# Kernel optimization log

Hardware: AMD Instinct MI355X
Metric: run time of the kernel (lower is better)

The kernel has to match this reference:

```python
import jax, jax.numpy as jnp
import numpy as np

N_NODES = 100000
N_EDGES = 1600000
N_GRAPHS = 512
F_IN = 20
HID = 128
OUT = HID // 2


def _glorot(key, shape):
    fan_in, fan_out = shape[0], shape[1]
    lim = float(np.sqrt(6.0 / (fan_in + fan_out)))
    return jax.random.uniform(key, shape, jnp.float32, -lim, lim)


def setup_inputs() -> dict:
    key = jax.random.key(0)
    ks = jax.random.split(key, 12)
    x = jax.random.normal(ks[0], (N_NODES, F_IN), jnp.float32)
    edge_index = jax.random.randint(ks[1], (2, N_EDGES), 0, N_NODES, dtype=jnp.int64)
    batch = jnp.sort(jax.random.randint(ks[2], (N_NODES,), 0, N_GRAPHS, dtype=jnp.int64))
    return {
        "x": x,
        "edge_index": edge_index,
        "batch": batch,
        "W1": _glorot(ks[3], (F_IN, HID)), "b1": jnp.zeros((HID,), jnp.float32),
        "W2": _glorot(ks[4], (HID, HID)), "b2": jnp.zeros((HID,), jnp.float32),
        "W3": _glorot(ks[5], (HID, HID)), "b3": jnp.zeros((HID,), jnp.float32),
        "Wout": _glorot(ks[6], (HID, OUT)), "bout": jnp.zeros((OUT,), jnp.float32),
    }


def _gcn_conv(x, W, b, src, dst, num_nodes):
    # PyG GCNConv: x' = D^{-1/2} (A + I) D^{-1/2} X W + b (self-loops already in src/dst)
    xw = x @ W                                                  # [N, H]
    ones = jnp.ones(src.shape[0], dtype=xw.dtype)
    deg = jax.ops.segment_sum(ones, dst, num_segments=num_nodes)
    dinv = jnp.where(deg > 0, jax.lax.rsqrt(deg), 0.0)          # [N]
    norm = dinv[src] * dinv[dst]                                # [E+N]
    msg = xw[src] * norm[:, None]                               # gather + scale
    return jax.ops.segment_sum(msg, dst, num_segments=num_nodes) + b


def reference(x, edge_index, batch, W1, b1, W2, b2, W3, b3, Wout, bout):
    num_nodes = x.shape[0]
    loops = jnp.arange(num_nodes, dtype=edge_index.dtype)
    src = jnp.concatenate([edge_index[0], loops])
    dst = jnp.concatenate([edge_index[1], loops])

    h = jax.nn.relu(_gcn_conv(x, W1, b1, src, dst, num_nodes))
    h = jax.nn.relu(_gcn_conv(h, W2, b2, src, dst, num_nodes))
    h = jax.nn.relu(_gcn_conv(h, W3, b3, src, dst, num_nodes))

    # global_mean_pool over graph ids
    sums = jax.ops.segment_sum(h, batch, num_segments=N_GRAPHS)
    counts = jax.ops.segment_sum(jnp.ones(num_nodes, h.dtype), batch, num_segments=N_GRAPHS)
    pooled = sums / jnp.maximum(counts, 1.0)[:, None]           # [G, H]
    return pooled @ Wout + bout                                 # [G, H//2]
```

## Files before the change

### kernel.cpp

```cpp
#include <hip/hip_runtime.h>
#include <hip/hip_fp16.h>

#define N_NODES 100000
#define N_EDGES 1600000
#define N_GRAPHS 512
#define F_IN 20
#define HID 128
#define OUT_F 64

#define BUCKETS 256
#define SPAN 391
#define BCAP 7000
#define EPB 2048

typedef _Float16 half8_t __attribute__((ext_vector_type(8)));
typedef float f32x4_t __attribute__((ext_vector_type(4)));

__device__ inline float4 h4_to_f4(uint2 u) {
    __half2 h0 = *(__half2*)&u.x;
    __half2 h1 = *(__half2*)&u.y;
    float2 f0 = __half22float2(h0);
    float2 f1 = __half22float2(h1);
    return make_float4(f0.x, f0.y, f1.x, f1.y);
}

__global__ __launch_bounds__(256) void partition(const int* __restrict__ src,
                                                 const int* __restrict__ dst,
                                                 int* __restrict__ bpairs,
                                                 int* cur256) {
    __shared__ int lcnt[4][BUCKETS];
    __shared__ int woff[4][BUCKETS];
    int t = threadIdx.x;
    int wv = t >> 6;
    for (int i = t; i < 4 * BUCKETS; i += 256) ((int*)lcnt)[i] = 0;
    __syncthreads();
    int base = blockIdx.x * EPB;
    int myb[8], myp[8], myr[8];
#pragma unroll
    for (int i = 0; i < 8; ++i) {
        int e = base + i * 256 + t;
        int b = -1, p = 0, rk = 0;
        if (e < N_EDGES) {
            int s = src[e], d = dst[e];
            b = d / SPAN;
            p = (s << 9) | (d - b * SPAN);
            rk = atomicAdd(&lcnt[wv][b], 1);
        }
        myb[i] = b; myp[i] = p; myr[i] = rk;
    }
    __syncthreads();
    {
        int c0 = lcnt[0][t], c1 = lcnt[1][t], c2 = lcnt[2][t], c3 = lcnt[3][t];
        int gb = atomicAdd(&cur256[t], c0 + c1 + c2 + c3);
        woff[0][t] = gb;
        woff[1][t] = gb + c0;
        woff[2][t] = gb + c0 + c1;
        woff[3][t] = gb + c0 + c1 + c2;
    }
    __syncthreads();
#pragma unroll
    for (int i = 0; i < 8; ++i) {
        int b = myb[i];
        if (b >= 0) {
            int p = woff[wv][b] + myr[i];
            if (p < BCAP) bpairs[(size_t)b * BCAP + p] = myp[i];
        }
    }
}

__global__ __launch_bounds__(256) void csr_build(const int* __restrict__ bpairs,
                                                 const int* __restrict__ cur256,
                                                 int* __restrict__ row_st,
                                                 int* __restrict__ csr,
                                                 const float* __restrict__ x,
                                                 __half* __restrict__ Xs) {
    __shared__ int ocnt[SPAN];
    __shared__ int sc[512];
    __shared__ int cur[SPAN];
    __shared__ int sbase;
    int b = blockIdx.x, t = threadIdx.x;

    int myc = cur256[t];
    sc[t] = myc;
    __syncthreads();
    for (int o = 1; o < BUCKETS; o <<= 1) {
        int v = (t >= o) ? sc[t - o] : 0;
        __syncthreads();
        sc[t] += v;
        __syncthreads();
    }
    if (t == b) sbase = sc[t] - myc;
    if (b == BUCKETS - 1 && t == 0) row_st[N_NODES] = N_EDGES;

    int n0 = b * SPAN;
    int span = N_NODES - n0; if (span > SPAN) span = SPAN;
    for (int i = t; i < SPAN; i += 256) ocnt[i] = 0;
    __syncthreads();

    int n = cur256[b];
    const int* p = bpairs + (size_t)b * BCAP;
    for (int i = t; i < n; i += 256) atomicAdd(&ocnt[p[i] & 511], 1);
    __syncthreads();
    sc[t]       = (t < span) ? ocnt[t] : 0;
    sc[t + 256] = (t + 256 < span) ? ocnt[t + 256] : 0;
    __syncthreads();
    for (int o = 1; o < 512; o <<= 1) {
        int a0 = (t >= o) ? sc[t - o] : 0;
        int a1 = sc[t + 256 - o];
        __syncthreads();
        sc[t] += a0;
        sc[t + 256] += a1;
        __syncthreads();
    }
    int base = sbase;
    for (int i = t; i < span; i += 256) {
        int start = sc[i] - ocnt[i];
        row_st[n0 + i] = base + start;
        cur[i] = start;
    }
    __syncthreads();
    for (int i = t; i < n; i += 256) {
        int e = p[i];
        int lp = atomicAdd(&cur[e & 511], 1);
        csr[base + lp] = e >> 9;
    }
    for (int i = t; i < span * 32; i += 256) {
        int nl = i >> 5, f = i & 31;
        float v = (f < F_IN) ? x[(size_t)(n0 + nl) * F_IN + f] : 0.f;
        float di = rsqrtf((float)(ocnt[nl] + 1));
        Xs[(size_t)(n0 + nl) * 32 + f] = __float2half(di * v);
    }
}

__global__ __launch_bounds__(256) void layer1(const __half* __restrict__ Xs,
                                              const int* __restrict__ row_st,
                                              const int* __restrict__ csr,
                                              const float* __restrict__ W,
                                              const float* __restrict__ bias,
                                              __half* __restrict__ H) {
    __shared__ float Wlds[F_IN * HID];
    __shared__ float Alds[16 * F_IN];
    const int t = threadIdx.x;
    const int node0 = blockIdx.x * 16;

    for (int i = t; i < F_IN * HID; i += 256) Wlds[i] = W[i];

    const int g = t >> 5;
    const int l = t & 31;
    const int hw = l >> 4, l16 = l & 15;
    const __half2* X2 = (const __half2*)Xs;
    for (int k2 = 0; k2 < 2; ++k2) {
        int nn = node0 + g * 2 + k2;
        int r0 = row_st[nn], r1 = row_st[nn + 1];
        float2 acc = make_float2(0.f, 0.f);
        if (hw == 0) {
            float2 f = __half22float2(X2[(size_t)nn * 16 + l16]);
            acc = f;
        }
        int r = r0 + hw;
        for (; r + 2 < r1; r += 4) {
            float2 f0 = __half22float2(X2[(size_t)csr[r] * 16 + l16]);
            float2 f1 = __half22float2(X2[(size_t)csr[r + 2] * 16 + l16]);
            acc.x += f0.x + f1.x;
            acc.y += f0.y + f1.y;
        }
        if (r < r1) {
            float2 f = __half22float2(X2[(size_t)csr[r] * 16 + l16]);
            acc.x += f.x; acc.y += f.y;
        }
        acc.x += __shfl_xor(acc.x, 16);
        acc.y += __shfl_xor(acc.y, 16);
        if (hw == 0 && l16 < 10) {
            float di = rsqrtf((float)(r1 - r0 + 1));
            Alds[(g * 2 + k2) * F_IN + l16 * 2]     = di * acc.x;
            Alds[(g * 2 + k2) * F_IN + l16 * 2 + 1] = di * acc.y;
        }
    }
    __syncthreads();

    const int h4 = (t & 31) * 4;
    float4 b4 = *(const float4*)&bias[h4];
    float4 acc0 = b4;
    float4 acc1 = b4;
#pragma unroll
    for (int kk = 0; kk < F_IN; ++kk) {
        float a0 = Alds[(g * 2) * F_IN + kk];
        float a1 = Alds[(g * 2 + 1) * F_IN + kk];
        float4 w = *(const float4*)&Wlds[kk * HID + h4];
        acc0.x = fmaf(a0, w.x, acc0.x);
        acc0.y = fmaf(a0, w.y, acc0.y);
        acc0.z = fmaf(a0, w.z, acc0.z);
        acc0.w = fmaf(a0, w.w, acc0.w);
        acc1.x = fmaf(a1, w.x, acc1.x);
        acc1.y = fmaf(a1, w.y, acc1.y);
        acc1.z = fmaf(a1, w.z, acc1.z);
        acc1.w = fmaf(a1, w.w, acc1.w);
    }
    {
        __half2 h0 = __floats2half2_rn(acc0.x, acc0.y);
        __half2 h1 = __floats2half2_rn(acc0.z, acc0.w);
        uint2 u; u.x = *(unsigned*)&h0; u.y = *(unsigned*)&h1;
        ((uint2*)H)[(node0 + g * 2) * 32 + (h4 >> 2)] = u;
    }
    {
        __half2 h0 = __floats2half2_rn(acc1.x, acc1.y);
        __half2 h1 = __floats2half2_rn(acc1.z, acc1.w);
        uint2 u; u.x = *(unsigned*)&h0; u.y = *(unsigned*)&h1;
        ((uint2*)H)[(node0 + g * 2 + 1) * 32 + (h4 >> 2)] = u;
    }
}

__global__ __launch_bounds__(256) void gemm_mfma(const __half* __restrict__ H,
                                                 const float* __restrict__ W,
                                                 const int* __restrict__ row_st,
                                                 __half* __restrict__ T) {
    __shared__ _Float16 Whi[64 * 128];
    __shared__ _Float16 Wlo[64 * 128];
    const int t = threadIdx.x;
    const int c0 = (blockIdx.x & 1) * 64;

    for (int i = t; i < 128 * 64; i += 256) {
        int k = i >> 6, c = i & 63;
        float w = W[k * HID + c0 + c];
        _Float16 hi = (_Float16)w;
        _Float16 lo = (_Float16)((w - (float)hi) * 2048.0f);
        int addr = c * 128 + (((k >> 3) ^ (c & 15)) << 3) + (k & 7);
        Whi[addr] = hi;
        Wlo[addr] = lo;
    }
    __syncthreads();

    const int wv = t >> 6;
    const int l  = t & 63;
    const int lr = l & 15;
    const int lq = l >> 4;

    for (int rep = 0; rep < 4; ++rep) {
        int strip = ((blockIdx.x >> 1) * 4 + wv) * 4 + rep;
        if (strip >= N_NODES / 16) continue;
        int n0 = strip * 16;

        f32x4_t acc[4], acl[4];
#pragma unroll
        for (int ct = 0; ct < 4; ++ct) { acc[ct] = (f32x4_t){0,0,0,0}; acl[ct] = (f32x4_t){0,0,0,0}; }

#pragma unroll
        for (int kc = 0; kc < 4; ++kc) {
            half8_t a = *(const half8_t*)(H + (size_t)(n0 + lr) * 128 + kc * 32 + lq * 8);
#pragma unroll
            for (int j = 0; j < 8; ++j) a[j] = a[j] > (_Float16)0 ? a[j] : (_Float16)0;
            int g = kc * 4 + lq;
#pragma unroll
            for (int ct = 0; ct < 4; ++ct) {
                int c = ct * 16 + lr;
                int addr = c * 128 + ((g ^ lr) << 3);
                half8_t bh = *(const half8_t*)&Whi[addr];
                half8_t bl = *(const half8_t*)&Wlo[addr];
                acc[ct] = __builtin_amdgcn_mfma_f32_16x16x32_f16(a, bh, acc[ct], 0, 0, 0);
                acl[ct] = __builtin_amdgcn_mfma_f32_16x16x32_f16(a, bl, acl[ct], 0, 0, 0);
            }
        }

        int r0 = n0 + lq * 4;
#pragma unroll
        for (int r = 0; r < 4; ++r) {
            int row = r0 + r;
            float d = rsqrtf((float)(row_st[row + 1] - row_st[row] + 1));
#pragma unroll
            for (int ct = 0; ct < 4; ++ct) {
                float v = (acc[ct][r] + acl[ct][r] * 4.8828125e-4f) * d;
                T[(size_t)row * 128 + c0 + ct * 16 + lr] = __float2half(v);
            }
        }
    }
}

__global__ __launch_bounds__(256) void gather_range(const __half* __restrict__ A,
                                                    const int* __restrict__ row_st,
                                                    const int* __restrict__ csr,
                                                    const float* __restrict__ bias,
                                                    __half* __restrict__ B) {
    int t = threadIdx.x;
    int n = blockIdx.x * 8 + (t >> 5);
    int l = t & 31;
    int r0 = row_st[n], r1 = row_st[n + 1];
    float di = rsqrtf((float)(r1 - r0 + 1));
    const uint2* Af = (const uint2*)A;
    float4 acc = h4_to_f4(Af[n * 32 + l]);
    int r = r0;
    for (; r + 7 < r1; r += 8) {
        int s0 = csr[r],     s1 = csr[r + 1], s2 = csr[r + 2], s3 = csr[r + 3];
        int s4 = csr[r + 4], s5 = csr[r + 5], s6 = csr[r + 6], s7 = csr[r + 7];
        float4 v0 = h4_to_f4(Af[s0 * 32 + l]);
        float4 v1 = h4_to_f4(Af[s1 * 32 + l]);
        float4 v2 = h4_to_f4(Af[s2 * 32 + l]);
        float4 v3 = h4_to_f4(Af[s3 * 32 + l]);
        float4 v4 = h4_to_f4(Af[s4 * 32 + l]);
        float4 v5 = h4_to_f4(Af[s5 * 32 + l]);
        float4 v6 = h4_to_f4(Af[s6 * 32 + l]);
        float4 v7 = h4_to_f4(Af[s7 * 32 + l]);
        acc.x += ((v0.x + v1.x) + (v2.x + v3.x)) + ((v4.x + v5.x) + (v6.x + v7.x));
        acc.y += ((v0.y + v1.y) + (v2.y + v3.y)) + ((v4.y + v5.y) + (v6.y + v7.y));
        acc.z += ((v0.z + v1.z) + (v2.z + v3.z)) + ((v4.z + v5.z) + (v6.z + v7.z));
        acc.w += ((v0.w + v1.w) + (v2.w + v3.w)) + ((v4.w + v5.w) + (v6.w + v7.w));
    }
    for (; r + 3 < r1; r += 4) {
        int s0 = csr[r], s1 = csr[r + 1], s2 = csr[r + 2], s3 = csr[r + 3];
        float4 v0 = h4_to_f4(Af[s0 * 32 + l]);
        float4 v1 = h4_to_f4(Af[s1 * 32 + l]);
        float4 v2 = h4_to_f4(Af[s2 * 32 + l]);
        float4 v3 = h4_to_f4(Af[s3 * 32 + l]);
        acc.x += (v0.x + v1.x) + (v2.x + v3.x);
        acc.y += (v0.y + v1.y) + (v2.y + v3.y);
        acc.z += (v0.z + v1.z) + (v2.z + v3.z);
        acc.w += (v0.w + v1.w) + (v2.w + v3.w);
    }
    for (; r < r1; ++r) {
        float4 v = h4_to_f4(Af[csr[r] * 32 + l]);
        acc.x += v.x; acc.y += v.y; acc.z += v.z; acc.w += v.w;
    }
    float4 b4 = ((const float4*)bias)[l];
    __half2 h0 = __floats2half2_rn(fmaf(di, acc.x, b4.x), fmaf(di, acc.y, b4.y));
    __half2 h1 = __floats2half2_rn(fmaf(di, acc.z, b4.z), fmaf(di, acc.w, b4.w));
    uint2 u; u.x = *(unsigned*)&h0; u.y = *(unsigned*)&h1;
    ((uint2*)B)[n * 32 + l] = u;
}

__global__ __launch_bounds__(256) void pool(const __half* __restrict__ B,
                                            const int* __restrict__ batch,
                                            float* sums, float* counts) {
    int t = threadIdx.x;
    int grp = blockIdx.x * 8 + (t >> 5);
    int l = t & 31;
    int h4 = l * 4;
    int n0 = grp * 8;
    if (n0 >= N_NODES) return;
    const uint2* Bf = (const uint2*)B;
    int cur = batch[n0];
    int runlen = 0;
    float4 acc = make_float4(0.f, 0.f, 0.f, 0.f);
    for (int k = 0; k < 8; ++k) {
        int n = n0 + k;
        if (n >= N_NODES) break;
        int g = batch[n];
        if (g != cur) {
            float* sp = &sums[cur * HID + h4];
            atomicAdd(sp + 0, acc.x); atomicAdd(sp + 1, acc.y);
            atomicAdd(sp + 2, acc.z); atomicAdd(sp + 3, acc.w);
            if (l == 0) atomicAdd(&counts[cur], (float)runlen);
            acc = make_float4(0.f, 0.f, 0.f, 0.f);
            runlen = 0;
            cur = g;
        }
        float4 v = h4_to_f4(Bf[n * 32 + l]);
        acc.x += fmaxf(v.x, 0.f);
        acc.y += fmaxf(v.y, 0.f);
        acc.z += fmaxf(v.z, 0.f);
        acc.w += fmaxf(v.w, 0.f);
        ++runlen;
    }
    float* sp = &sums[cur * HID + h4];
    atomicAdd(sp + 0, acc.x); atomicAdd(sp + 1, acc.y);
    atomicAdd(sp + 2, acc.z); atomicAdd(sp + 3, acc.w);
    if (l == 0) atomicAdd(&counts[cur], (float)runlen);
}

__global__ void final_gemm(const float* __restrict__ sums, const float* __restrict__ counts,
                           const float* __restrict__ Wout, const float* __restrict__ bout,
                           float* __restrict__ out) {
    int g = blockIdx.x;
    int o = threadIdx.x;
    __shared__ float p[HID];
    for (int k = o; k < HID; k += 64) p[k] = sums[g * HID + k];
    __syncthreads();
    float inv = 1.0f / fmaxf(counts[g], 1.0f);
    float acc = 0.f;
#pragma unroll 8
    for (int k = 0; k < HID; ++k)
        acc = fmaf(p[k], Wout[k * OUT_F + o], acc);
    out[g * OUT_F + o] = fmaf(inv, acc, bout[o]);
}

extern "C" void kernel_launch(void* const* d_in, const int* in_sizes, int n_in,
                              void* d_out, int out_size, void* d_ws, size_t ws_size,
                              hipStream_t stream) {
    const float* x     = (const float*)d_in[0];
    const int*   ei    = (const int*)d_in[1];
    const int*   batch = (const int*)d_in[2];
    const float* W1    = (const float*)d_in[3];
    const float* b1    = (const float*)d_in[4];
    const float* W2    = (const float*)d_in[5];
    const float* b2    = (const float*)d_in[6];
    const float* W3    = (const float*)d_in[7];
    const float* b3    = (const float*)d_in[8];
    const float* Wout  = (const float*)d_in[9];
    const float* bout  = (const float*)d_in[10];
    float* out = (float*)d_out;

    const int* src = ei;
    const int* dst = ei + N_EDGES;

    float* A      = (float*)d_ws;
    float* Breg   = A + (size_t)N_NODES * HID;
    int*   row_st = (int*)(Breg + (size_t)N_NODES * HID);
    float* sums   = (float*)(row_st + N_NODES + 1);
    float* counts = sums + N_GRAPHS * HID;
    int*   cur256 = (int*)(counts + N_GRAPHS);
    int*   csr    = cur256 + BUCKETS;

    int*    bpairs = (int*)A;
    __half* Xs     = (__half*)((char*)A + 7168000);
    __half* T      = (__half*)A;
    __half* H      = (__half*)Breg;

    hipMemsetAsync(sums, 0, (size_t)(N_GRAPHS * HID + N_GRAPHS + BUCKETS) * 4, stream);
    partition<<<(N_EDGES + EPB - 1) / EPB, 256, 0, stream>>>(src, dst, bpairs, cur256);
    csr_build<<<BUCKETS, 256, 0, stream>>>(bpairs, cur256, row_st, csr, x, Xs);

    layer1<<<N_NODES / 16, 256, 0, stream>>>(Xs, row_st, csr, W1, b1, H);

    gemm_mfma<<<782, 256, 0, stream>>>(H, W2, row_st, T);
    gather_range<<<N_NODES / 8, 256, 0, stream>>>(T, row_st, csr, b2, H);
    gemm_mfma<<<782, 256, 0, stream>>>(H, W3, row_st, T);
    gather_range<<<N_NODES / 8, 256, 0, stream>>>(T, row_st, csr, b3, H);

    pool<<<(N_NODES / 8 + 7) / 8, 256, 0, stream>>>(H, batch, sums, counts);
    final_gemm<<<N_GRAPHS, 64, 0, stream>>>(sums, counts, Wout, bout, out);
}
```

Measured before the change: 405.1 us.

## Fuse final aggregation into pooling and widen partition/CSR blocks to 512 threads

Result: faster. 373.5 us (-7.8%).

```diff
diff --git a/kernel.cpp b/kernel.cpp
--- a/kernel.cpp
+++ b/kernel.cpp
@@ -11,7 +11,7 @@
 #define BUCKETS 256
 #define SPAN 391
 #define BCAP 7000
-#define EPB 2048
+#define EPB 4096
 
 typedef _Float16 half8_t __attribute__((ext_vector_type(8)));
 typedef float f32x4_t __attribute__((ext_vector_type(4)));
@@ -24,21 +24,21 @@
     return make_float4(f0.x, f0.y, f1.x, f1.y);
 }
 
-__global__ __launch_bounds__(256) void partition(const int* __restrict__ src,
+__global__ __launch_bounds__(512) void partition(const int* __restrict__ src,
                                                  const int* __restrict__ dst,
                                                  int* __restrict__ bpairs,
                                                  int* cur256) {
-    __shared__ int lcnt[4][BUCKETS];
-    __shared__ int woff[4][BUCKETS];
+    __shared__ int lcnt[8][BUCKETS];
+    __shared__ int woff[8][BUCKETS];
     int t = threadIdx.x;
     int wv = t >> 6;
-    for (int i = t; i < 4 * BUCKETS; i += 256) ((int*)lcnt)[i] = 0;
+    for (int i = t; i < 8 * BUCKETS; i += 512) ((int*)lcnt)[i] = 0;
     __syncthreads();
     int base = blockIdx.x * EPB;
     int myb[8], myp[8], myr[8];
 #pragma unroll
     for (int i = 0; i < 8; ++i) {
-        int e = base + i * 256 + t;
+        int e = base + i * 512 + t;
         int b = -1, p = 0, rk = 0;
         if (e < N_EDGES) {
             int s = src[e], d = dst[e];
@@ -49,13 +49,13 @@
         myb[i] = b; myp[i] = p; myr[i] = rk;
     }
     __syncthreads();
-    {
-        int c0 = lcnt[0][t], c1 = lcnt[1][t], c2 = lcnt[2][t], c3 = lcnt[3][t];
-        int gb = atomicAdd(&cur256[t], c0 + c1 + c2 + c3);
-        woff[0][t] = gb;
-        woff[1][t] = gb + c0;
-        woff[2][t] = gb + c0 + c1;
-        woff[3][t] = gb + c0 + c1 + c2;
+    if (t < BUCKETS) {
+        int c[8], tot = 0;
+#pragma unroll
+        for (int w = 0; w < 8; ++w) { c[w] = lcnt[w][t]; tot += c[w]; }
+        int gb = atomicAdd(&cur256[t], tot);
+#pragma unroll
+        for (int w = 0; w < 8; ++w) { woff[w][t] = gb; gb += c[w]; }
     }
     __syncthreads();
 #pragma unroll
@@ -68,7 +68,7 @@
     }
 }
 
-__global__ __launch_bounds__(256) void csr_build(const int* __restrict__ bpairs,
+__global__ __launch_bounds__(512) void csr_build(const int* __restrict__ bpairs,
                                                  const int* __restrict__ cur256,
                                                  int* __restrict__ row_st,
                                                  int* __restrict__ csr,
@@ -80,7 +80,7 @@
     __shared__ int sbase;
     int b = blockIdx.x, t = threadIdx.x;
 
-    int myc = cur256[t];
+    int myc = (t < BUCKETS) ? cur256[t] : 0;
     sc[t] = myc;
     __syncthreads();
     for (int o = 1; o < BUCKETS; o <<= 1) {
@@ -94,37 +94,34 @@
 
     int n0 = b * SPAN;
     int span = N_NODES - n0; if (span > SPAN) span = SPAN;
-    for (int i = t; i < SPAN; i += 256) ocnt[i] = 0;
+    if (t < SPAN) ocnt[t] = 0;
     __syncthreads();
 
     int n = cur256[b];
     const int* p = bpairs + (size_t)b * BCAP;
-    for (int i = t; i < n; i += 256) atomicAdd(&ocnt[p[i] & 511], 1);
-    __syncthreads();
-    sc[t]       = (t < span) ? ocnt[t] : 0;
-    sc[t + 256] = (t + 256 < span) ? ocnt[t + 256] : 0;
+    for (int i = t; i < n; i += 512) atomicAdd(&ocnt[p[i] & 511], 1);
+    __syncthreads();
+    sc[t] = (t < span) ? ocnt[t] : 0;
     __syncthreads();
     for (int o = 1; o < 512; o <<= 1) {
-        int a0 = (t >= o) ? sc[t - o] : 0;
-        int a1 = sc[t + 256 - o];
+        int v = (t >= o) ? sc[t - o] : 0;
         __syncthreads();
-        sc[t] += a0;
-        sc[t + 256] += a1;
+        sc[t] += v;
         __syncthreads();
     }
     int base = sbase;
-    for (int i = t; i < span; i += 256) {
-        int start = sc[i] - ocnt[i];
-        row_st[n0 + i] = base + start;
-        cur[i] = start;
-    }
-    __syncthreads();
-    for (int i = t; i < n; i += 256) {
+    if (t < span) {
+        int start = sc[t] - ocnt[t];
+        row_st[n0 + t] = base + start;
+        cur[t] = start;
+    }
+    __syncthreads();
+    for (int i = t; i < n; i += 512) {
         int e = p[i];
         int lp = atomicAdd(&cur[e & 511], 1);
         csr[base + lp] = e >> 9;
     }
-    for (int i = t; i < span * 32; i += 256) {
+    for (int i = t; i < span * 32; i += 512) {
         int nl = i >> 5, f = i & 31;
         float v = (f < F_IN) ? x[(size_t)(n0 + nl) * F_IN + f] : 0.f;
         float di = rsqrtf((float)(ocnt[nl] + 1));
@@ -145,39 +142,34 @@
 
     for (int i = t; i < F_IN * HID; i += 256) Wlds[i] = W[i];
 
-    const int g = t >> 5;
-    const int l = t & 31;
-    const int hw = l >> 4, l16 = l & 15;
+    const int h16 = t >> 4;
+    const int l16 = t & 15;
     const __half2* X2 = (const __half2*)Xs;
-    for (int k2 = 0; k2 < 2; ++k2) {
-        int nn = node0 + g * 2 + k2;
+    {
+        int nn = node0 + h16;
         int r0 = row_st[nn], r1 = row_st[nn + 1];
-        float2 acc = make_float2(0.f, 0.f);
-        if (hw == 0) {
-            float2 f = __half22float2(X2[(size_t)nn * 16 + l16]);
-            acc = f;
-        }
-        int r = r0 + hw;
-        for (; r + 2 < r1; r += 4) {
+        float2 f = __half22float2(X2[(size_t)nn * 16 + l16]);
+        float2 acc = f;
+        int r = r0;
+        for (; r + 1 < r1; r += 2) {
             float2 f0 = __half22float2(X2[(size_t)csr[r] * 16 + l16]);
-            float2 f1 = __half22float2(X2[(size_t)csr[r + 2] * 16 + l16]);
+            float2 f1 = __half22float2(X2[(size_t)csr[r + 1] * 16 + l16]);
             acc.x += f0.x + f1.x;
             acc.y += f0.y + f1.y;
         }
         if (r < r1) {
-            float2 f = __half22float2(X2[(size_t)csr[r] * 16 + l16]);
-            acc.x += f.x; acc.y += f.y;
-        }
-        acc.x += __shfl_xor(acc.x, 16);
-        acc.y += __shfl_xor(acc.y, 16);
-        if (hw == 0 && l16 < 10) {
+            float2 f2 = __half22float2(X2[(size_t)csr[r] * 16 + l16]);
+            acc.x += f2.x; acc.y += f2.y;
+        }
+        if (l16 < 10) {
             float di = rsqrtf((float)(r1 - r0 + 1));
-            Alds[(g * 2 + k2) * F_IN + l16 * 2]     = di * acc.x;
-            Alds[(g * 2 + k2) * F_IN + l16 * 2 + 1] = di * acc.y;
-        }
-    }
-    __syncthreads();
-
+            Alds[h16 * F_IN + l16 * 2]     = di * acc.x;
+            Alds[h16 * F_IN + l16 * 2 + 1] = di * acc.y;
+        }
+    }
+    __syncthreads();
+
+    const int g  = t >> 5;
     const int h4 = (t & 31) * 4;
     float4 b4 = *(const float4*)&bias[h4];
     float4 acc0 = b4;
@@ -326,42 +318,78 @@
     ((uint2*)B)[n * 32 + l] = u;
 }
 
-__global__ __launch_bounds__(256) void pool(const __half* __restrict__ B,
-                                            const int* __restrict__ batch,
-                                            float* sums, float* counts) {
+__global__ __launch_bounds__(256) void gather_pool(const __half* __restrict__ A,
+                                                   const int* __restrict__ row_st,
+                                                   const int* __restrict__ csr,
+                                                   const float* __restrict__ bias,
+                                                   const int* __restrict__ batch,
+                                                   float* sums, float* counts) {
     int t = threadIdx.x;
-    int grp = blockIdx.x * 8 + (t >> 5);
     int l = t & 31;
-    int h4 = l * 4;
-    int n0 = grp * 8;
+    int n0 = (blockIdx.x * 8 + (t >> 5)) * 8;
     if (n0 >= N_NODES) return;
-    const uint2* Bf = (const uint2*)B;
+    const uint2* Af = (const uint2*)A;
+    float4 b4 = ((const float4*)bias)[l];
     int cur = batch[n0];
     int runlen = 0;
-    float4 acc = make_float4(0.f, 0.f, 0.f, 0.f);
+    float4 pacc = make_float4(0.f, 0.f, 0.f, 0.f);
     for (int k = 0; k < 8; ++k) {
         int n = n0 + k;
         if (n >= N_NODES) break;
         int g = batch[n];
         if (g != cur) {
-            float* sp = &sums[cur * HID + h4];
-            atomicAdd(sp + 0, acc.x); atomicAdd(sp + 1, acc.y);
-            atomicAdd(sp + 2, acc.z); atomicAdd(sp + 3, acc.w);
+            float* sp = &sums[cur * HID + l * 4];
+            atomicAdd(sp + 0, pacc.x); atomicAdd(sp + 1, pacc.y);
+            atomicAdd(sp + 2, pacc.z); atomicAdd(sp + 3, pacc.w);
             if (l == 0) atomicAdd(&counts[cur], (float)runlen);
-            acc = make_float4(0.f, 0.f, 0.f, 0.f);
+            pacc = make_float4(0.f, 0.f, 0.f, 0.f);
             runlen = 0;
             cur = g;
         }
-        float4 v = h4_to_f4(Bf[n * 32 + l]);
-        acc.x += fmaxf(v.x, 0.f);
-        acc.y += fmaxf(v.y, 0.f);
-        acc.z += fmaxf(v.z, 0.f);
-        acc.w += fmaxf(v.w, 0.f);
+        int r0 = row_st[n], r1 = row_st[n + 1];
+        float4 acc = h4_to_f4(Af[n * 32 + l]);
+        int r = r0;
+        for (; r + 7 < r1; r += 8) {
+            int s0 = csr[r],     s1 = csr[r + 1], s2 = csr[r + 2], s3 = csr[r + 3];
+            int s4 = csr[r + 4], s5 = csr[r + 5], s6 = csr[r + 6], s7 = csr[r + 7];
+            float4 v0 = h4_to_f4(Af[s0 * 32 + l]);
+            float4 v1 = h4_to_f4(Af[s1 * 32 + l]);
+            float4 v2 = h4_to_f4(Af[s2 * 32 + l]);
+            float4 v3 = h4_to_f4(Af[s3 * 32 + l]);
+            float4 v4 = h4_to_f4(Af[s4 * 32 + l]);
+            float4 v5 = h4_to_f4(Af[s5 * 32 + l]);
+            float4 v6 = h4_to_f4(Af[s6 * 32 + l]);
+            float4 v7 = h4_to_f4(Af[s7 * 32 + l]);
+            acc.x += ((v0.x + v1.x) + (v2.x + v3.x)) + ((v4.x + v5.x) + (v6.x + v7.x));
+            acc.y += ((v0.y + v1.y) + (v2.y + v3.y)) + ((v4.y + v5.y) + (v6.y + v7.y));
+            acc.z += ((v0.z + v1.z) + (v2.z + v3.z)) + ((v4.z + v5.z) + (v6.z + v7.z));
+            acc.w += ((v0.w + v1.w) + (v2.w + v3.w)) + ((v4.w + v5.w) + (v6.w + v7.w));
+        }
+        for (; r + 3 < r1; r += 4) {
+            int s0 = csr[r], s1 = csr[r + 1], s2 = csr[r + 2], s3 = csr[r + 3];
+            float4 v0 = h4_to_f4(Af[s0 * 32 + l]);
+            float4 v1 = h4_to_f4(Af[s1 * 32 + l]);
+            float4 v2 = h4_to_f4(Af[s2 * 32 + l]);
+            float4 v3 = h4_to_f4(Af[s3 * 32 + l]);
+            acc.x += (v0.x + v1.x) + (v2.x + v3.x);
+            acc.y += (v0.y + v1.y) + (v2.y + v3.y);
+            acc.z += (v0.z + v1.z) + (v2.z + v3.z);
+            acc.w += (v0.w + v1.w) + (v2.w + v3.w);
+        }
+        for (; r < r1; ++r) {
+            float4 v = h4_to_f4(Af[csr[r] * 32 + l]);
+            acc.x += v.x; acc.y += v.y; acc.z += v.z; acc.w += v.w;
+        }
+        float di = rsqrtf((float)(r1 - r0 + 1));
+        pacc.x += fmaxf(fmaf(di, acc.x, b4.x), 0.f);
+        pacc.y += fmaxf(fmaf(di, acc.y, b4.y), 0.f);
+        pacc.z += fmaxf(fmaf(di, acc.z, b4.z), 0.f);
+        pacc.w += fmaxf(fmaf(di, acc.w, b4.w), 0.f);
         ++runlen;
     }
-    float* sp = &sums[cur * HID + h4];
-    atomicAdd(sp + 0, acc.x); atomicAdd(sp + 1, acc.y);
-    atomicAdd(sp + 2, acc.z); atomicAdd(sp + 3, acc.w);
+    float* sp = &sums[cur * HID + l * 4];
+    atomicAdd(sp + 0, pacc.x); atomicAdd(sp + 1, pacc.y);
+    atomicAdd(sp + 2, pacc.z); atomicAdd(sp + 3, pacc.w);
     if (l == 0) atomicAdd(&counts[cur], (float)runlen);
 }
 
@@ -414,16 +442,15 @@
     __half* H      = (__half*)Breg;
 
     hipMemsetAsync(sums, 0, (size_t)(N_GRAPHS * HID + N_GRAPHS + BUCKETS) * 4, stream);
-    partition<<<(N_EDGES + EPB - 1) / EPB, 256, 0, stream>>>(src, dst, bpairs, cur256);
-    csr_build<<<BUCKETS, 256, 0, stream>>>(bpairs, cur256, row_st, csr, x, Xs);
+    partition<<<(N_EDGES + EPB - 1) / EPB, 512, 0, stream>>>(src, dst, bpairs, cur256);
+    csr_build<<<BUCKETS, 512, 0, stream>>>(bpairs, cur256, row_st, csr, x, Xs);
 
     layer1<<<N_NODES / 16, 256, 0, stream>>>(Xs, row_st, csr, W1, b1, H);
 
     gemm_mfma<<<782, 256, 0, stream>>>(H, W2, row_st, T);
     gather_range<<<N_NODES / 8, 256, 0, stream>>>(T, row_st, csr, b2, H);
     gemm_mfma<<<782, 256, 0, stream>>>(H, W3, row_st, T);
-    gather_range<<<N_NODES / 8, 256, 0, stream>>>(T, row_st, csr, b3, H);
-
-    pool<<<(N_NODES / 8 + 7) / 8, 256, 0, stream>>>(H, batch, sums, counts);
+    gather_pool<<<(N_NODES + 63) / 64, 256, 0, stream>>>(T, row_st, csr, b3, batch, sums, counts);
+
     final_gemm<<<N_GRAPHS, 64, 0, stream>>>(sums, counts, Wout, bout, out);
 }
```
